# Optimization experiments

Measured on AMD Instinct MI355X. Metric: run time of the kernel, lower is better.

## Reference

```python
import jax, jax.numpy as jnp
import numpy as np

N_CODES = 16384
EMB_DIM = 256
BETA = 0.25


def setup_inputs() -> dict:
    key = jax.random.key(0)
    k1, k2 = jax.random.split(key)
    z = jax.random.normal(k1, (8, EMB_DIM, 32, 32), dtype=jnp.float32)
    # embedding init: uniform(-1/n_codes, 1/n_codes)
    emb = jax.random.uniform(k2, (N_CODES, EMB_DIM), dtype=jnp.float32,
                             minval=-1.0 / N_CODES, maxval=1.0 / N_CODES)
    return {"z": z, "emb": emb}


def reference(z, emb):
    # z: [B, C, H, W] -> [B, H, W, C]
    z_nhwc = jnp.transpose(z, (0, 2, 3, 1))
    zf = z_nhwc.reshape(-1, EMB_DIM)  # [N, D]
    # squared distances ||z||^2 + ||e||^2 - 2 z.e   -> [N, n_codes]
    d = (jnp.sum(zf * zf, axis=1, keepdims=True)
         + jnp.sum(emb * emb, axis=1)
         - 2.0 * jnp.einsum('nd,kd->nk', zf, emb))
    idx = jnp.argmin(d, axis=1)  # [N]
    z_q = emb[idx].reshape(z_nhwc.shape)  # [B, H, W, C]
    sg = jax.lax.stop_gradient
    loss = jnp.mean((sg(z_q) - z_nhwc) ** 2) + BETA * jnp.mean((z_q - sg(z_nhwc)) ** 2)
    # straight-through estimator
    z_q = z_nhwc + sg(z_q - z_nhwc)
    z_q = jnp.transpose(z_q, (0, 3, 1, 2))  # back to NCHW
    return z_q, loss, idx
```

## Files before the change

### kernel.cpp

```cpp
#include <hip/hip_runtime.h>
#include <hip/hip_fp16.h>

#define DIM 256
#define MARGIN 2.25e-4f

typedef __bf16 bf8v __attribute__((ext_vector_type(8)));
typedef float f4v __attribute__((ext_vector_type(4)));

__device__ inline unsigned short f2bf(float x) {
    unsigned u = __float_as_uint(x);
    u += 0x7fffu + ((u >> 16) & 1u);
    return (unsigned short)(u >> 16);
}

__global__ __launch_bounds__(256) void k_prep(const float* __restrict__ z,
                                              const float* __restrict__ emb,
                                              float* __restrict__ zf,
                                              unsigned short* __restrict__ zb,
                                              unsigned short* __restrict__ eb,
                                              float* __restrict__ enorm,
                                              float* __restrict__ out_loss) {
    const int bx = blockIdx.x;
    if (bx < 2048) {
        __shared__ float tt[32][33];
        const int hw0 = (bx & 31) * 32;
        const int d0  = ((bx >> 5) & 7) * 32;
        const int b   = bx >> 8;
        const int tx = threadIdx.x & 31, ty = threadIdx.x >> 5;
#pragma unroll
        for (int i = 0; i < 4; i++) {
            const int d = d0 + ty + 8 * i;
            tt[ty + 8 * i][tx] = z[(b * 256 + d) * 1024 + hw0 + tx];
        }
        __syncthreads();
#pragma unroll
        for (int i = 0; i < 4; i++) {
            const int hw = hw0 + ty + 8 * i;
            const float v = tt[tx][ty + 8 * i];
            const size_t o = (size_t)(b * 1024 + hw) * DIM + d0 + tx;
            zf[o] = v;
            zb[o] = f2bf(v);
        }
    } else if (bx < 6144) {
        const int s = bx - 2048;
        const int wave = threadIdx.x >> 6, lane = threadIdx.x & 63;
        const int row = s * 4 + wave;
        const float4 v = *(const float4*)(emb + (size_t)row * DIM + lane * 4);
        ushort4 o;
        o.x = f2bf(v.x); o.y = f2bf(v.y); o.z = f2bf(v.z); o.w = f2bf(v.w);
        const int g = row >> 4, m = row & 15;
        const int kk = lane >> 3, qq = (lane >> 1) & 3, e = (lane & 1) * 4;
        *(ushort4*)(eb + (size_t)(g * 8 + kk) * 512 + qq * 128 + m * 8 + e) = o;
        float ss = v.x * v.x + v.y * v.y + v.z * v.z + v.w * v.w;
#pragma unroll
        for (int m2 = 1; m2 < 64; m2 <<= 1) ss += __shfl_xor(ss, m2, 64);
        if (lane == 0) enorm[row] = ss;
    } else {
        if (threadIdx.x == 0) out_loss[0] = 0.f;
    }
}

#define GLOADB(dst, voff, base) \
    asm volatile("global_load_dwordx4 %0, %1, %2" : "=&v"(dst) : "v"(voff), "s"(base))
#define SO(KK) ((unsigned)((((KK) >> 3) * 131072) + (((KK) & 7) * 1024)))

#define ISSUE(sl, KK) \
    GLOADB(Bp##sl##_0, voffb0 + SO(KK), eb); \
    GLOADB(Bp##sl##_1, voffb1 + SO(KK), eb); \
    GLOADB(Bp##sl##_2, voffb2 + SO(KK), eb); \
    GLOADB(Bp##sl##_3, voffb3 + SO(KK), eb);

#define MFMA4(rt, AF, sl) \
    acc[rt][0] = __builtin_amdgcn_mfma_f32_16x16x32_bf16(AF, Bp##sl##_0, acc[rt][0], 0, 0, 0); \
    acc[rt][1] = __builtin_amdgcn_mfma_f32_16x16x32_bf16(AF, Bp##sl##_1, acc[rt][1], 0, 0, 0); \
    acc[rt][2] = __builtin_amdgcn_mfma_f32_16x16x32_bf16(AF, Bp##sl##_2, acc[rt][2], 0, 0, 0); \
    acc[rt][3] = __builtin_amdgcn_mfma_f32_16x16x32_bf16(AF, Bp##sl##_3, acc[rt][3], 0, 0, 0);

#define STEP(kk, sl, wv) { \
    asm volatile("s_waitcnt vmcnt(" #wv ")" ::: "memory"); \
    __builtin_amdgcn_sched_barrier(0); \
    const int slot_ = (((kk) * 4 + q) ^ m15) * 8; \
    const bf8v af0 = *(const bf8v*)&As[(m15)      * 256 + slot_]; \
    const bf8v af1 = *(const bf8v*)&As[(16 + m15) * 256 + slot_]; \
    const bf8v af2 = *(const bf8v*)&As[(32 + m15) * 256 + slot_]; \
    const bf8v af3 = *(const bf8v*)&As[(48 + m15) * 256 + slot_]; \
    __builtin_amdgcn_s_setprio(1); \
    MFMA4(0, af0, sl) \
    MFMA4(1, af1, sl) \
    MFMA4(2, af2, sl) \
    MFMA4(3, af3, sl) \
    __builtin_amdgcn_s_setprio(0); }

#define EPI(pp) { \
    const int by_ = nb * 4 + (pp); \
    const int gsl_ = wc * 4 + (m15 >> 2); \
    const float e0_ = en_lds[(pp) * 256 + wc * 64 +  0 + m15]; \
    const float e1_ = en_lds[(pp) * 256 + wc * 64 + 16 + m15]; \
    const float e2_ = en_lds[(pp) * 256 + wc * 64 + 32 + m15]; \
    const float e3_ = en_lds[(pp) * 256 + wc * 64 + 48 + m15]; \
    _Pragma("unroll") \
    for (int rt = 0; rt < 4; rt++) { \
        float sv[4]; \
        _Pragma("unroll") \
        for (int j = 0; j < 4; j++) { \
            float s_ = fmaf(-2.f, acc[rt][0][j], e0_); \
            s_ = fminf(s_, fmaf(-2.f, acc[rt][1][j], e1_)); \
            s_ = fminf(s_, fmaf(-2.f, acc[rt][2][j], e2_)); \
            s_ = fminf(s_, fmaf(-2.f, acc[rt][3][j], e3_)); \
            sv[j] = s_; \
        } \
        _Pragma("unroll") \
        for (int m = 1; m <= 2; m <<= 1) { \
            _Pragma("unroll") \
            for (int j = 0; j < 4; j++) sv[j] = fminf(sv[j], __shfl_xor(sv[j], m, 64)); \
        } \
        if ((m15 & 3) == 0) { \
            const int rl_ = rt * 16 + q * 4; \
            _Pragma("unroll") \
            for (int j = 0; j < 4; j++) \
                sm[(rl_ + j) * 16 + gsl_] = __half_as_ushort(__float2half_rn(sv[j])); \
        } \
    } \
    asm volatile("s_waitcnt lgkmcnt(0)" ::: "memory"); \
    __builtin_amdgcn_sched_barrier(0); \
    __builtin_amdgcn_s_barrier(); \
    __builtin_amdgcn_sched_barrier(0); \
    if (t < 128) { \
        const uint4 v_ = *(const uint4*)&sm[t * 8]; \
        *(uint4*)&pvalh[(size_t)(row0 + (t >> 1)) * 1024 + by_ * 16 + (t & 1) * 8] = v_; \
    } \
    __builtin_amdgcn_sched_barrier(0); \
    __builtin_amdgcn_s_barrier(); \
    __builtin_amdgcn_sched_barrier(0); \
    _Pragma("unroll") \
    for (int rt = 0; rt < 4; rt++) { \
        _Pragma("unroll") \
        for (int ct = 0; ct < 4; ct++) acc[rt][ct] = (f4v){0.f, 0.f, 0.f, 0.f}; \
    } }

__global__ __launch_bounds__(256, 3) void k_score(
        const unsigned short* __restrict__ zb, const unsigned short* __restrict__ eb,
        const float* __restrict__ enorm, unsigned short* __restrict__ pvalh) {
    __shared__ unsigned short As[64 * 256];
    __shared__ unsigned short sm[64 * 16];
    __shared__ float en_lds[1024];
    const int bid = blockIdx.x;
    const int rx = (bid >> 3) & 127;
    const int nb = ((bid >> 10) << 3) + (bid & 7);
    const int row0 = rx * 64;
    const int t = threadIdx.x;
    const int lane = t & 63, wc = t >> 6;
    const int q = lane >> 4, m15 = lane & 15;

#pragma unroll
    for (int j = 0; j < 8; j++) {
        const int id = j * 256 + t;
        const int r = id >> 5, sl = id & 31;
        const int c = sl ^ (r & 15);
        __builtin_amdgcn_global_load_lds(
            (const __attribute__((address_space(1))) void*)(zb + (size_t)(row0 + r) * DIM + c * 8),
            (__attribute__((address_space(3))) void*)((char*)As + id * 16), 16, 0, 0);
    }
#pragma unroll
    for (int j = 0; j < 4; j++) {
        __builtin_amdgcn_global_load_lds(
            (const __attribute__((address_space(1))) void*)(enorm + nb * 1024 + j * 256 + t),
            (__attribute__((address_space(3))) void*)((char*)en_lds + (j * 256 + t) * 4), 4, 0, 0);
    }
    __syncthreads();

    f4v acc[4][4];
#pragma unroll
    for (int rt = 0; rt < 4; rt++)
#pragma unroll
        for (int ct = 0; ct < 4; ct++) acc[rt][ct] = (f4v){0.f, 0.f, 0.f, 0.f};

    const unsigned voffb0 = (unsigned)((nb * 64 + wc * 4 + 0) * 8192 + lane * 16);
    const unsigned voffb1 = (unsigned)((nb * 64 + wc * 4 + 1) * 8192 + lane * 16);
    const unsigned voffb2 = (unsigned)((nb * 64 + wc * 4 + 2) * 8192 + lane * 16);
    const unsigned voffb3 = (unsigned)((nb * 64 + wc * 4 + 3) * 8192 + lane * 16);

    bf8v Bp0_0, Bp0_1, Bp0_2, Bp0_3;
    bf8v Bp1_0, Bp1_1, Bp1_2, Bp1_3;
    bf8v Bp2_0, Bp2_1, Bp2_2, Bp2_3;

    ISSUE(0, 0) ISSUE(1, 1) ISSUE(2, 2)

    STEP(0, 0, 8) ISSUE(0, 3)
    STEP(1, 1, 8) ISSUE(1, 4)
    STEP(2, 2, 8) ISSUE(2, 5)
    STEP(3, 0, 8) ISSUE(0, 6)
    STEP(4, 1, 8) ISSUE(1, 7)
    STEP(5, 2, 8) ISSUE(2, 8)
    STEP(6, 0, 8) ISSUE(0, 9)
    STEP(7, 1, 8) ISSUE(1, 10)
    EPI(0)
    STEP(0, 2, 8) ISSUE(2, 11)
    STEP(1, 0, 8) ISSUE(0, 12)
    STEP(2, 1, 8) ISSUE(1, 13)
    STEP(3, 2, 8) ISSUE(2, 14)
    STEP(4, 0, 8) ISSUE(0, 15)
    STEP(5, 1, 8) ISSUE(1, 16)
    STEP(6, 2, 8) ISSUE(2, 17)
    STEP(7, 0, 8) ISSUE(0, 18)
    EPI(1)
    STEP(0, 1, 8) ISSUE(1, 19)
    STEP(1, 2, 8) ISSUE(2, 20)
    STEP(2, 0, 8) ISSUE(0, 21)
    STEP(3, 1, 8) ISSUE(1, 22)
    STEP(4, 2, 8) ISSUE(2, 23)
    STEP(5, 0, 8) ISSUE(0, 24)
    STEP(6, 1, 8) ISSUE(1, 25)
    STEP(7, 2, 8) ISSUE(2, 26)
    EPI(2)
    STEP(0, 0, 8) ISSUE(0, 27)
    STEP(1, 1, 8) ISSUE(1, 28)
    STEP(2, 2, 8) ISSUE(2, 29)
    STEP(3, 0, 8) ISSUE(0, 30)
    STEP(4, 1, 8) ISSUE(1, 31)
    STEP(5, 2, 8)
    STEP(6, 0, 4)
    STEP(7, 1, 0)
    EPI(3)
}

__global__ __launch_bounds__(256) void k_select(
        const float* __restrict__ zf, const float* __restrict__ emb,
        const float* __restrict__ enorm, const unsigned short* __restrict__ pvalh,
        int* __restrict__ idxi, float* __restrict__ out_idx) {
    const int row = blockIdx.x;
    const int t = threadIdx.x;
    const int lane = t & 63, w = t >> 6;
    __shared__ float zs[256];
    __shared__ float wred[4];
    __shared__ int lcnt;
    __shared__ int list[1024];
    __shared__ float fs[16];
    __shared__ int fi[16];

    const float zv = zf[(size_t)row * DIM + t];
    zs[t] = zv;
    if (t == 0) lcnt = 0;
    float nrm = zv * zv;
#pragma unroll
    for (int m = 1; m < 64; m <<= 1) nrm += __shfl_xor(nrm, m, 64);
    if (lane == 0) wred[w] = nrm;

    const __half* p = (const __half*)(pvalh + (size_t)row * 1024 + t * 4);
    float v[4];
#pragma unroll
    for (int k = 0; k < 4; k++) v[k] = __half2float(p[k]);
    float mn = fminf(fminf(v[0], v[1]), fminf(v[2], v[3]));
#pragma unroll
    for (int m = 1; m < 64; m <<= 1) mn = fminf(mn, __shfl_xor(mn, m, 64));
    __shared__ float wmin[4];
    if (lane == 0) wmin[w] = mn;
    __syncthreads();
    const float zn = wred[0] + wred[1] + wred[2] + wred[3];
    const float g = fminf(fminf(wmin[0], wmin[1]), fminf(wmin[2], wmin[3])) + MARGIN;
#pragma unroll
    for (int k = 0; k < 4; k++) {
        if (v[k] <= g) {
            const int pos = atomicAdd(&lcnt, 1);
            list[pos] = t * 4 + k;
        }
    }
    __syncthreads();

    const int lane16 = t & 15, codei = t >> 4;
    const int n = lcnt;
    float bv = 3.0e38f;
    int bi = 0x7fffffff;
    for (int i = 0; i < n; i++) {
        const int gg = list[i];
        const int cbase = ((gg >> 4) << 8) + (((gg >> 2) & 3) << 6) + ((gg & 3) << 2);
        const int code = cbase + ((codei >> 2) << 4) + (codei & 3);
        const float* zp = zs + lane16 * 16;
        const float* ep = emb + (size_t)code * DIM + lane16 * 16;
        float d = 0.f;
#pragma unroll
        for (int k = 0; k < 16; k += 4) {
            const float4 ev = *(const float4*)(ep + k);
            const float4 zv4 = *(const float4*)(zp + k);
            d = fmaf(zv4.x, ev.x, d);
            d = fmaf(zv4.y, ev.y, d);
            d = fmaf(zv4.z, ev.z, d);
            d = fmaf(zv4.w, ev.w, d);
        }
#pragma unroll
        for (int m = 1; m <= 8; m <<= 1) d += __shfl_xor(d, m, 64);
        if (lane16 == 0) {
            const float tt = zn + enorm[code];
            const float s = tt - 2.0f * d;
            if (s < bv || (s == bv && code < bi)) { bv = s; bi = code; }
        }
    }
    if (lane16 == 0) { fs[codei] = bv; fi[codei] = bi; }
    __syncthreads();
    if (t == 0) {
        float b = fs[0]; int c = fi[0];
#pragma unroll
        for (int k = 1; k < 16; k++)
            if (fs[k] < b || (fs[k] == b && fi[k] < c)) { b = fs[k]; c = fi[k]; }
        idxi[row] = c;
        out_idx[row] = (float)c;
    }
}

__global__ __launch_bounds__(256) void k_gather(const float* __restrict__ emb,
                                                const float* __restrict__ zf,
                                                const int* __restrict__ idxi,
                                                float* __restrict__ zq,
                                                float* __restrict__ out_loss) {
    __shared__ float t[32][33];
    const int hw0 = blockIdx.x * 32;
    const int c0  = blockIdx.y * 32;
    const int b   = blockIdx.z;
    const int tx = threadIdx.x & 31, ty = threadIdx.x >> 5;
    float lsum = 0.f;
#pragma unroll
    for (int i = 0; i < 4; i++) {
        const int hh = ty + 8 * i;
        const int n = b * 1024 + hw0 + hh;
        const int id = idxi[n];
        const float q = emb[(size_t)id * DIM + c0 + tx];
        const float zv = zf[(size_t)n * DIM + c0 + tx];
        const float d = q - zv;
        lsum += d * d;
        t[hh][tx] = q;
    }
    __syncthreads();
#pragma unroll
    for (int i = 0; i < 4; i++) {
        const int c = c0 + ty + 8 * i;
        zq[(size_t)(b * 256 + c) * 1024 + hw0 + tx] = t[tx][ty + 8 * i];
    }
#pragma unroll
    for (int m = 1; m < 64; m <<= 1) lsum += __shfl_xor(lsum, m, 64);
    __shared__ float wsum[4];
    const int lane = threadIdx.x & 63, w = threadIdx.x >> 6;
    if (lane == 0) wsum[w] = lsum;
    __syncthreads();
    if (threadIdx.x == 0) {
        const float total = wsum[0] + wsum[1] + wsum[2] + wsum[3];
        atomicAdd(out_loss, total * (1.25f / 2097152.0f));
    }
}

extern "C" void kernel_launch(void* const* d_in, const int* in_sizes, int n_in,
                              void* d_out, int out_size, void* d_ws, size_t ws_size,
                              hipStream_t stream) {
    const float* z   = (const float*)d_in[0];
    const float* emb = (const float*)d_in[1];
    float* out = (float*)d_out;
    float* ws  = (float*)d_ws;

    float*          zf    = ws;
    unsigned short* pvalh = (unsigned short*)(ws + 2097152);
    unsigned short* zb    = (unsigned short*)(ws + 6291456);
    unsigned short* eb    = (unsigned short*)(ws + 7340032);
    float*          enorm = ws + 9437184;
    int*            idxi  = (int*)(ws + 9453568);

    float* zq       = out;
    float* out_loss = out + 2097152;
    float* out_idx  = out + 2097153;

    k_prep<<<dim3(6145), 256, 0, stream>>>(z, emb, zf, zb, eb, enorm, out_loss);
    k_score<<<dim3(2048), 256, 0, stream>>>(zb, eb, enorm, pvalh);
    k_select<<<dim3(8192), 256, 0, stream>>>(zf, emb, enorm, pvalh, idxi, out_idx);
    k_gather<<<dim3(32, 8, 8), 256, 0, stream>>>(emb, zf, idxi, zq, out_loss);
}
```

Baseline: 218.5 us.

## Double-buffer LDS A-fragments and cut B prefetch depth from three to two

Restructures the GEMM main loop so the A fragments for the next k-step are read from LDS into a second register set while the MFMAs for the current step run, overlapping LDS latency with matrix math. At the same time it shrinks the global B-tile prefetch ring from three slots to two, which frees registers for the extra A buffers. The cost is less global-load latency hiding, since only one step of B loads is in flight ahead of use, which could stall on HBM/L2 latency.

```diff
diff --git a/kernel.cpp b/kernel.cpp
--- a/kernel.cpp
+++ b/kernel.cpp
@@ -76,20 +76,24 @@
     acc[rt][2] = __builtin_amdgcn_mfma_f32_16x16x32_bf16(AF, Bp##sl##_2, acc[rt][2], 0, 0, 0); \
     acc[rt][3] = __builtin_amdgcn_mfma_f32_16x16x32_bf16(AF, Bp##sl##_3, acc[rt][3], 0, 0, 0);
 
-#define STEP(kk, sl, wv) { \
-    asm volatile("s_waitcnt vmcnt(" #wv ")" ::: "memory"); \
-    __builtin_amdgcn_sched_barrier(0); \
+#define PF(dp, kk) { \
     const int slot_ = (((kk) * 4 + q) ^ m15) * 8; \
-    const bf8v af0 = *(const bf8v*)&As[(m15)      * 256 + slot_]; \
-    const bf8v af1 = *(const bf8v*)&As[(16 + m15) * 256 + slot_]; \
-    const bf8v af2 = *(const bf8v*)&As[(32 + m15) * 256 + slot_]; \
-    const bf8v af3 = *(const bf8v*)&As[(48 + m15) * 256 + slot_]; \
+    Af##dp##_0 = *(const bf8v*)&As[(m15)      * 256 + slot_]; \
+    Af##dp##_1 = *(const bf8v*)&As[(16 + m15) * 256 + slot_]; \
+    Af##dp##_2 = *(const bf8v*)&As[(32 + m15) * 256 + slot_]; \
+    Af##dp##_3 = *(const bf8v*)&As[(48 + m15) * 256 + slot_]; }
+
+#define CMP(P, sl) \
     __builtin_amdgcn_s_setprio(1); \
-    MFMA4(0, af0, sl) \
-    MFMA4(1, af1, sl) \
-    MFMA4(2, af2, sl) \
-    MFMA4(3, af3, sl) \
-    __builtin_amdgcn_s_setprio(0); }
+    MFMA4(0, Af##P##_0, sl) \
+    MFMA4(1, Af##P##_1, sl) \
+    MFMA4(2, Af##P##_2, sl) \
+    MFMA4(3, Af##P##_3, sl) \
+    __builtin_amdgcn_s_setprio(0);
+
+#define WV(n) { asm volatile("s_waitcnt vmcnt(" #n ")" ::: "memory"); \
+                __builtin_amdgcn_sched_barrier(0); }
+#define SB __builtin_amdgcn_sched_barrier(0);
 
 #define EPI(pp) { \
     const int by_ = nb * 4 + (pp); \
@@ -182,45 +186,47 @@
 
     bf8v Bp0_0, Bp0_1, Bp0_2, Bp0_3;
     bf8v Bp1_0, Bp1_1, Bp1_2, Bp1_3;
-    bf8v Bp2_0, Bp2_1, Bp2_2, Bp2_3;
-
-    ISSUE(0, 0) ISSUE(1, 1) ISSUE(2, 2)
-
-    STEP(0, 0, 8) ISSUE(0, 3)
-    STEP(1, 1, 8) ISSUE(1, 4)
-    STEP(2, 2, 8) ISSUE(2, 5)
-    STEP(3, 0, 8) ISSUE(0, 6)
-    STEP(4, 1, 8) ISSUE(1, 7)
-    STEP(5, 2, 8) ISSUE(2, 8)
-    STEP(6, 0, 8) ISSUE(0, 9)
-    STEP(7, 1, 8) ISSUE(1, 10)
+    bf8v Af0_0, Af0_1, Af0_2, Af0_3;
+    bf8v Af1_0, Af1_1, Af1_2, Af1_3;
+
+    ISSUE(0, 0) ISSUE(1, 1)
+    PF(0, 0)
+
+    WV(4) PF(1, 1) SB CMP(0, 0) ISSUE(0, 2)
+    WV(4) PF(0, 2) SB CMP(1, 1) ISSUE(1, 3)
+    WV(4) PF(1, 3) SB CMP(0, 0) ISSUE(0, 4)
+    WV(4) PF(0, 4) SB CMP(1, 1) ISSUE(1, 5)
+    WV(4) PF(1, 5) SB CMP(0, 0) ISSUE(0, 6)
+    WV(4) PF(0, 6) SB CMP(1, 1) ISSUE(1, 7)
+    WV(4) PF(1, 7) SB CMP(0, 0) ISSUE(0, 8)
+    WV(4) PF(0, 0) SB CMP(1, 1) ISSUE(1, 9)
     EPI(0)
-    STEP(0, 2, 8) ISSUE(2, 11)
-    STEP(1, 0, 8) ISSUE(0, 12)
-    STEP(2, 1, 8) ISSUE(1, 13)
-    STEP(3, 2, 8) ISSUE(2, 14)
-    STEP(4, 0, 8) ISSUE(0, 15)
-    STEP(5, 1, 8) ISSUE(1, 16)
-    STEP(6, 2, 8) ISSUE(2, 17)
-    STEP(7, 0, 8) ISSUE(0, 18)
+    WV(4) PF(1, 1) SB CMP(0, 0) ISSUE(0, 10)
+    WV(4) PF(0, 2) SB CMP(1, 1) ISSUE(1, 11)
+    WV(4) PF(1, 3) SB CMP(0, 0) ISSUE(0, 12)
+    WV(4) PF(0, 4) SB CMP(1, 1) ISSUE(1, 13)
+    WV(4) PF(1, 5) SB CMP(0, 0) ISSUE(0, 14)
+    WV(4) PF(0, 6) SB CMP(1, 1) ISSUE(1, 15)
+    WV(4) PF(1, 7) SB CMP(0, 0) ISSUE(0, 16)
+    WV(4) PF(0, 0) SB CMP(1, 1) ISSUE(1, 17)
     EPI(1)
-    STEP(0, 1, 8) ISSUE(1, 19)
-    STEP(1, 2, 8) ISSUE(2, 20)
-    STEP(2, 0, 8) ISSUE(0, 21)
-    STEP(3, 1, 8) ISSUE(1, 22)
-    STEP(4, 2, 8) ISSUE(2, 23)
-    STEP(5, 0, 8) ISSUE(0, 24)
-    STEP(6, 1, 8) ISSUE(1, 25)
-    STEP(7, 2, 8) ISSUE(2, 26)
+    WV(4) PF(1, 1) SB CMP(0, 0) ISSUE(0, 18)
+    WV(4) PF(0, 2) SB CMP(1, 1) ISSUE(1, 19)
+    WV(4) PF(1, 3) SB CMP(0, 0) ISSUE(0, 20)
+    WV(4) PF(0, 4) SB CMP(1, 1) ISSUE(1, 21)
+    WV(4) PF(1, 5) SB CMP(0, 0) ISSUE(0, 22)
+    WV(4) PF(0, 6) SB CMP(1, 1) ISSUE(1, 23)
+    WV(4) PF(1, 7) SB CMP(0, 0) ISSUE(0, 24)
+    WV(4) PF(0, 0) SB CMP(1, 1) ISSUE(1, 25)
     EPI(2)
-    STEP(0, 0, 8) ISSUE(0, 27)
-    STEP(1, 1, 8) ISSUE(1, 28)
-    STEP(2, 2, 8) ISSUE(2, 29)
-    STEP(3, 0, 8) ISSUE(0, 30)
-    STEP(4, 1, 8) ISSUE(1, 31)
-    STEP(5, 2, 8)
-    STEP(6, 0, 4)
-    STEP(7, 1, 0)
+    WV(4) PF(1, 1) SB CMP(0, 0) ISSUE(0, 26)
+    WV(4) PF(0, 2) SB CMP(1, 1) ISSUE(1, 27)
+    WV(4) PF(1, 3) SB CMP(0, 0) ISSUE(0, 28)
+    WV(4) PF(0, 4) SB CMP(1, 1) ISSUE(1, 29)
+    WV(4) PF(1, 5) SB CMP(0, 0) ISSUE(0, 30)
+    WV(4) PF(0, 6) SB CMP(1, 1) ISSUE(1, 31)
+    WV(4) PF(1, 7) SB CMP(0, 0)
+    WV(0)          SB CMP(1, 1)
     EPI(3)
 }
 
```

Result: no change. 215.9 us (-1.2%).
